# Performance work log

Hardware: AMD Instinct MI355X
Metric: run time of the kernel (lower is better)

The kernel has to match this reference:

```python
import jax, jax.numpy as jnp
import numpy as np

N_ITERS = 200   # fixed PDHG iterations (stands in for SCS max_iters)
POWER_ITERS = 30


def setup_inputs() -> dict:
    key = jax.random.key(0)
    k1, k2 = jax.random.split(key)
    B, n_hos, n_types, n_structs = 512, 16, 16, 4096
    m = n_hos * n_types
    # bids (capacities) are strictly positive counts
    X = jax.random.uniform(k1, (B, n_hos, n_types), jnp.float32, minval=1.0, maxval=10.0)
    # sparse 0/1 cycle-incidence matrix (each column = one feasible exchange structure)
    S = (jax.random.uniform(k2, (m, n_structs)) < 0.03).astype(jnp.float32)
    return {"X": X, "S": S, "batch_size": B}


def _solve_lp_batch(S, b, n_iters=N_ITERS):
    """Batched LP:  max 1^T x  s.t.  x >= 0,  S x <= b,  via Chambolle-Pock PDHG.

    S: [m, n] shared constraint matrix; b: [B, m] per-sample rhs.
    Returns x: [B, n] (the allocation that CvxpyLayer/SCS would return).
    """
    m, n = S.shape
    B = b.shape[0]
    w = jnp.ones((B, n), b.dtype)

    # spectral norm of S via power iteration -> step sizes
    v = jnp.ones((n,), S.dtype)

    def pw(v, _):
        v = S.T @ (S @ v)
        return v / jnp.linalg.norm(v), None

    v, _ = jax.lax.scan(pw, v, None, length=POWER_ITERS)
    L = jnp.sqrt(jnp.vdot(v, S.T @ (S @ v)))  # ~ ||S||_2
    tau = 0.9 / L
    sigma = 0.9 / L

    x0 = jnp.zeros((B, n), b.dtype)
    y0 = jnp.zeros((B, m), b.dtype)  # dual for Sx <= b

    def step(carry, _):
        x, y = carry
        # primal: gradient ascent on w^T x - y^T S x, projected to x >= 0
        x_new = jnp.maximum(x + tau * (w - y @ S), 0.0)        # [B,n]
        # dual: ascent on constraint residual with extrapolated primal, y >= 0
        y_new = jnp.maximum(y + sigma * ((2.0 * x_new - x) @ S.T - b), 0.0)  # [B,m]
        return (x_new, y_new), None

    (x, _), _ = jax.lax.scan(step, (x0, y0), None, length=n_iters)
    return x


def reference(X, S, batch_size):
    m, _ = S.shape
    b = X.reshape(batch_size, m)  # B = X.view(batch, n_hos*n_types)
    return _solve_lp_batch(S, b)  # [batch, n_structures]
```

## Files before the change

kernel.cpp:

```cpp
#include <hip/hip_runtime.h>

#define M 256
#define N 4096
#define NIT 200
#define PIT 30
#define CSRCAP 131072

#define YDUMMY (256*8)
#define ZDUMMY (4096*8)

__global__ void k_colcnt(const float* __restrict__ S, int* __restrict__ col_cnt){
  int j = blockIdx.x*256 + threadIdx.x;
  int c = 0;
  for (int i = 0; i < M; ++i) c += (S[i*N + j] != 0.0f) ? 1 : 0;
  col_cnt[j] = c;
}

__global__ void k_rowcnt(const float* __restrict__ S, int* __restrict__ row_cnt){
  int wid = blockIdx.x*(blockDim.x>>6) + (threadIdx.x>>6);
  int l = threadIdx.x & 63;
  if (wid >= M) return;
  int cnt = 0;
  for (int jc = 0; jc < N/64; ++jc){
    float v = S[wid*N + jc*64 + l];
    unsigned long long mask = __ballot(v != 0.0f);
    cnt += __popcll(mask);
  }
  if (l == 0) row_cnt[wid] = cnt;
}

__global__ void k_sortcol(const int* __restrict__ col_cnt,
                          int* __restrict__ col_perm, int* __restrict__ col_rank){
  __shared__ int cs[N];
  int t0 = threadIdx.x;
  for (int t = 0; t < N/256; ++t) cs[t0 + 256*t] = col_cnt[t0 + 256*t];
  __syncthreads();
  int j = blockIdx.x*256 + t0;
  int cj = cs[j];
  int rank = 0;
  #pragma unroll 4
  for (int jj = 0; jj < N; ++jj){
    int c = cs[jj];
    rank += ((c < cj) || (c == cj && jj < j)) ? 1 : 0;
  }
  col_perm[rank] = j;
  col_rank[j] = rank;
}

__global__ void k_sortrow(const int* __restrict__ row_cnt,
                          int* __restrict__ row_perm, int* __restrict__ row_ptr){
  int i = threadIdx.x;
  int ci = row_cnt[i];
  int rank = 0, pre = 0;
  for (int ii = 0; ii < M; ++ii){
    int c = row_cnt[ii];
    bool less = (c < ci) || (c == ci && ii < i);
    rank += less ? 1 : 0;
    pre  += less ? c : 0;
  }
  row_perm[rank] = i;
  row_ptr[rank]  = pre;
}

__global__ void k_fillcsr(const float* __restrict__ S, const int* __restrict__ row_perm,
                          const int* __restrict__ row_ptr, unsigned short* __restrict__ csr){
  int rr = blockIdx.x*(blockDim.x>>6) + (threadIdx.x>>6);
  int l = threadIdx.x & 63;
  if (rr >= M) return;
  int i = row_perm[rr];
  int pos = row_ptr[rr];
  for (int jc = 0; jc < N/64; ++jc){
    float v = S[i*N + jc*64 + l];
    unsigned long long mask = __ballot(v != 0.0f);
    if (v != 0.0f){
      int off = __popcll(mask & ((1ull << l) - 1ull));
      int p = pos + off;
      if (p < CSRCAP) csr[p] = (unsigned short)((jc*64 + l)*8);
    }
    pos += __popcll(mask);
  }
}

__global__ void k_trips(const int* __restrict__ col_cnt, const int* __restrict__ col_perm,
                        const int* __restrict__ row_cnt, const int* __restrict__ row_perm,
                        int* __restrict__ pT4, int* __restrict__ pB4,
                        int* __restrict__ dT4, int* __restrict__ dB4){
  int tid = threadIdx.x;
  if (tid < 64){
    int k = tid >> 4, w = tid & 15;
    int mx = 0;
    for (int l = 0; l < 64; ++l){
      int s = 64*w + l + 1024*k;
      int c = col_cnt[col_perm[s]];
      mx = max(mx, c);
    }
    pT4[tid] = min((mx + 3) >> 2, 16);
  } else if (tid < 80){
    int w = tid - 64;
    int mx = 0;
    for (int l = 0; l < 64; ++l){
      int t = w*64 + l;
      int r = t >> 2, q = t & 3;
      int len = row_cnt[row_perm[r]];
      int qs = (len*q) >> 2, qe = (len*(q+1)) >> 2;
      mx = max(mx, qe - qs);
    }
    dT4[w] = min((mx + 3) >> 2, 80);
  }
  __syncthreads();
  if (tid == 0){
    int acc = 0;
    for (int i = 0; i < 64; ++i){ pB4[i] = acc; acc += pT4[i]; }
    acc = 0;
    for (int i = 0; i < 16; ++i){ dB4[i] = acc; acc += dT4[i]; }
  }
}

__global__ void k_fillp(const float* __restrict__ S, const int* __restrict__ col_rank,
                        const int* __restrict__ pT4, const int* __restrict__ pB4,
                        unsigned short* __restrict__ pstream){
  int j = blockIdx.x*256 + threadIdx.x;
  int s = col_rank[j];
  int k = s >> 10, rem = s & 1023, w = rem >> 6, l = rem & 63;
  int kw = k*16 + w;
  int base = pB4[kw];
  int cap = pT4[kw]*4;
  int t = 0;
  for (int i = 0; i < M && t < cap; ++i){
    if (S[i*N + j] != 0.0f){
      pstream[((base + (t>>2))*64 + l)*4 + (t&3)] = (unsigned short)(i*8);
      ++t;
    }
  }
  for (; t < cap; ++t)
    pstream[((base + (t>>2))*64 + l)*4 + (t&3)] = (unsigned short)YDUMMY;
}

__global__ void k_filld(const unsigned short* __restrict__ csr,
                        const int* __restrict__ row_cnt, const int* __restrict__ row_perm,
                        const int* __restrict__ row_ptr,
                        const int* __restrict__ dT4, const int* __restrict__ dB4,
                        unsigned short* __restrict__ dstream){
  int tid = blockIdx.x*256 + threadIdx.x;
  int w = tid >> 6, l = tid & 63;
  int r = tid >> 2, q = tid & 3;
  int len = row_cnt[row_perm[r]];
  int rb = row_ptr[r];
  int qs = (len*q) >> 2, qe = (len*(q+1)) >> 2;
  int base = dB4[w];
  int cap = dT4[w]*4;
  int qlen = qe - qs; if (qlen > cap) qlen = cap;
  int t = 0;
  for (; t < qlen; ++t)
    dstream[((base + (t>>2))*64 + l)*4 + (t&3)] = csr[rb + qs + t];
  for (; t < cap; ++t)
    dstream[((base + (t>>2))*64 + l)*4 + (t&3)] = (unsigned short)ZDUMMY;
}

__global__ __launch_bounds__(1024) void k_power(
    const ushort4* __restrict__ pstream, const ushort4* __restrict__ dstream,
    const int* __restrict__ col_perm, const int* __restrict__ row_perm,
    const int* __restrict__ pT4, const int* __restrict__ pB4,
    const int* __restrict__ dT4, const int* __restrict__ dB4,
    float* __restrict__ tauw)
{
  __shared__ float2 v_s[N+8];
  __shared__ float2 u_s[M+8];
  __shared__ float2 red2[1024];
  const int tid = threadIdx.x, w = tid >> 6, l = tid & 63;

  int cj[4], pb[4], pt[4];
  float tl[4];
  #pragma unroll
  for (int k = 0; k < 4; ++k){
    int kw = k*16 + w;
    pb[k] = pB4[kw]; pt[k] = pT4[kw];
    cj[k] = col_perm[tid + 1024*k];
    v_s[cj[k]] = make_float2(1.0f, 0.0f);
    tl[k] = 0.0f;
  }
  const int r = tid >> 2, q = tid & 3;
  const int rid = row_perm[r];
  const int db = dB4[w], dt = dT4[w];
  if (tid < 8){ v_s[N+tid] = make_float2(0,0); u_s[M+tid] = make_float2(0,0); }
  __syncthreads();

  const char* vb = (const char*)v_s;
  const char* ub = (const char*)u_s;

  for (int it = 0; it < PIT; ++it){
    float a = 0.0f;
    for (int c = 0; c < dt; ++c){
      ushort4 ix = dstream[(db + c)*64 + l];
      a += ((const float2*)(vb + ix.x))->x + ((const float2*)(vb + ix.y))->x
         + ((const float2*)(vb + ix.z))->x + ((const float2*)(vb + ix.w))->x;
    }
    a += __shfl_xor(a, 1);
    a += __shfl_xor(a, 2);
    if (q == 0) u_s[rid] = make_float2(a, 0.0f);
    __syncthreads();
    #pragma unroll
    for (int k = 0; k < 4; ++k){
      float a2 = 0.0f;
      for (int c = 0; c < pt[k]; ++c){
        ushort4 ix = pstream[(pb[k] + c)*64 + l];
        a2 += ((const float2*)(ub + ix.x))->x + ((const float2*)(ub + ix.y))->x
            + ((const float2*)(ub + ix.z))->x + ((const float2*)(ub + ix.w))->x;
      }
      tl[k] = a2 * (1.0f/1024.0f);
      v_s[cj[k]] = make_float2(tl[k], 0.0f);
    }
    __syncthreads();
  }

  float pv = 0.0f;
  #pragma unroll
  for (int k = 0; k < 4; ++k) pv += tl[k]*tl[k];
  float a = 0.0f;
  for (int c = 0; c < dt; ++c){
    ushort4 ix = dstream[(db + c)*64 + l];
    a += ((const float2*)(vb + ix.x))->x + ((const float2*)(vb + ix.y))->x
       + ((const float2*)(vb + ix.z))->x + ((const float2*)(vb + ix.w))->x;
  }
  a += __shfl_xor(a, 1);
  a += __shfl_xor(a, 2);
  float fsq = (q == 0) ? a*a : 0.0f;
  red2[tid] = make_float2(pv, fsq);
  __syncthreads();
  for (int sd = 512; sd > 0; sd >>= 1){
    if (tid < sd){
      red2[tid].x += red2[tid+sd].x;
      red2[tid].y += red2[tid+sd].y;
    }
    __syncthreads();
  }
  if (tid == 0) tauw[0] = 0.9f * sqrtf(red2[0].x / red2[0].y);
}

__global__ __launch_bounds__(1024) void k_main(
    const float* __restrict__ X,
    const ushort4* __restrict__ pstream, const ushort4* __restrict__ dstream,
    const int* __restrict__ col_perm, const int* __restrict__ row_perm,
    const int* __restrict__ pT4, const int* __restrict__ pB4,
    const int* __restrict__ dT4, const int* __restrict__ dB4,
    const float* __restrict__ tauw, float* __restrict__ out)
{
  __shared__ float2 z_s[N+8];
  __shared__ float2 y_s[M+8];
  const int tid = threadIdx.x, w = tid >> 6, l = tid & 63;
  const int b0 = blockIdx.x * 2;
  const float tau = tauw[0];
  const float sigma = tau;

  int cj[4], pb[4], pt[4];
  float2 x[4];
  #pragma unroll
  for (int k = 0; k < 4; ++k){
    int kw = k*16 + w;
    pb[k] = pB4[kw]; pt[k] = pT4[kw];
    cj[k] = col_perm[tid + 1024*k];
    x[k] = make_float2(0.0f, 0.0f);
  }
  const int r = tid >> 2, q = tid & 3;
  const int rid = row_perm[r];
  const int db = dB4[w], dt = dT4[w];
  float2 bi = make_float2(0,0), yv = make_float2(0,0);
  if (q == 0){
    bi.x = X[b0*M + rid];
    bi.y = X[(b0+1)*M + rid];
    y_s[rid] = make_float2(0,0);
  }
  if (tid < 8){ y_s[M+tid] = make_float2(0,0); z_s[N+tid] = make_float2(0,0); }
  __syncthreads();

  const char* yb = (const char*)y_s;
  const char* zb = (const char*)z_s;

  for (int it = 0; it < NIT; ++it){
    const bool last = (it == NIT-1);
    #pragma unroll
    for (int k = 0; k < 4; ++k){
      float ax = 0.0f, ay = 0.0f;
      for (int c = 0; c < pt[k]; ++c){
        ushort4 ix = pstream[(pb[k] + c)*64 + l];
        float2 a0 = *(const float2*)(yb + ix.x);
        float2 a1 = *(const float2*)(yb + ix.y);
        float2 a2 = *(const float2*)(yb + ix.z);
        float2 a3 = *(const float2*)(yb + ix.w);
        ax += (a0.x + a1.x) + (a2.x + a3.x);
        ay += (a0.y + a1.y) + (a2.y + a3.y);
      }
      float2 xo = x[k];
      float xnx = fmaxf(xo.x + tau*(1.0f - ax), 0.0f);
      float xny = fmaxf(xo.y + tau*(1.0f - ay), 0.0f);
      if (!last) z_s[cj[k]] = make_float2(2.0f*xnx - xo.x, 2.0f*xny - xo.y);
      x[k] = make_float2(xnx, xny);
    }
    if (last) break;
    __syncthreads();
    float ax = 0.0f, ay = 0.0f;
    for (int c = 0; c < dt; ++c){
      ushort4 ix = dstream[(db + c)*64 + l];
      float2 a0 = *(const float2*)(zb + ix.x);
      float2 a1 = *(const float2*)(zb + ix.y);
      float2 a2 = *(const float2*)(zb + ix.z);
      float2 a3 = *(const float2*)(zb + ix.w);
      ax += (a0.x + a1.x) + (a2.x + a3.x);
      ay += (a0.y + a1.y) + (a2.y + a3.y);
    }
    ax += __shfl_xor(ax, 1);  ay += __shfl_xor(ay, 1);
    ax += __shfl_xor(ax, 2);  ay += __shfl_xor(ay, 2);
    if (q == 0){
      yv.x = fmaxf(yv.x + sigma*(ax - bi.x), 0.0f);
      yv.y = fmaxf(yv.y + sigma*(ay - bi.y), 0.0f);
      y_s[rid] = yv;
    }
    __syncthreads();
  }

  #pragma unroll
  for (int k = 0; k < 4; ++k){
    out[(size_t)b0*N + cj[k]]     = x[k].x;
    out[(size_t)(b0+1)*N + cj[k]] = x[k].y;
  }
}

extern "C" void kernel_launch(void* const* d_in, const int* in_sizes, int n_in,
                              void* d_out, int out_size, void* d_ws, size_t ws_size,
                              hipStream_t stream)
{
  const float* X = (const float*)d_in[0];
  const float* S = (const float*)d_in[1];
  float* out = (float*)d_out;
  const int B = in_sizes[0] / M;

  char* p = (char*)d_ws;
  auto alloc = [&](size_t bytes)->char*{
    char* q = p; p += (bytes + 255) & ~size_t(255); return q;
  };
  int* col_cnt  = (int*)alloc(N*sizeof(int));
  int* col_perm = (int*)alloc(N*sizeof(int));
  int* col_rank = (int*)alloc(N*sizeof(int));
  int* row_cnt  = (int*)alloc(M*sizeof(int));
  int* row_perm = (int*)alloc(M*sizeof(int));
  int* row_ptr  = (int*)alloc(M*sizeof(int));
  int* pT4      = (int*)alloc(64*sizeof(int));
  int* pB4      = (int*)alloc(64*sizeof(int));
  int* dT4      = (int*)alloc(16*sizeof(int));
  int* dB4      = (int*)alloc(16*sizeof(int));
  float* tauw   = (float*)alloc(256);
  unsigned short* csr     = (unsigned short*)alloc(CSRCAP*sizeof(unsigned short));
  unsigned short* pstream = (unsigned short*)alloc(65536ull*8);
  unsigned short* dstream = (unsigned short*)alloc(81920ull*8);

  k_colcnt <<<N/256, 256, 0, stream>>>(S, col_cnt);
  k_rowcnt <<<16, 1024, 0, stream>>>(S, row_cnt);
  k_sortcol<<<N/256, 256, 0, stream>>>(col_cnt, col_perm, col_rank);
  k_sortrow<<<1, M, 0, stream>>>(row_cnt, row_perm, row_ptr);
  k_fillcsr<<<16, 1024, 0, stream>>>(S, row_perm, row_ptr, csr);
  k_trips  <<<1, 256, 0, stream>>>(col_cnt, col_perm, row_cnt, row_perm, pT4, pB4, dT4, dB4);
  k_fillp  <<<N/256, 256, 0, stream>>>(S, col_rank, pT4, pB4, pstream);
  k_filld  <<<4, 256, 0, stream>>>(csr, row_cnt, row_perm, row_ptr, dT4, dB4, dstream);
  k_power  <<<1, 1024, 0, stream>>>((const ushort4*)pstream, (const ushort4*)dstream,
                                    col_perm, row_perm, pT4, pB4, dT4, dB4, tauw);
  k_main   <<<B/2, 1024, 0, stream>>>(X, (const ushort4*)pstream, (const ushort4*)dstream,
                                      col_perm, row_perm, pT4, pB4, dT4, dB4, tauw, out);
}
```

Before: 1.332 ms.

## Replicate dual vector across LDS banks and fuse power iteration into main kernel

The dual vector y is now stored 32 times in shared memory (one copy per bank slot), and each pstream index is rewritten to point at a lane-specific replica. Gathers in the primal step then spread across banks instead of colliding. One slot per row is left unwritten and kept at zero so it can act as the padding target. The separate single-block power-iteration kernel is removed, and every main block recomputes the spectral norm itself, which removes a serial launch at the cost of redundant work in all blocks and heavier shared-memory use (64KB for y_rep).

Measured after the change: 1.412 ms. 1.06x slower.

```diff
diff --git a/kernel.cpp b/kernel.cpp
--- a/kernel.cpp
+++ b/kernel.cpp
@@ -6,8 +6,7 @@
 #define PIT 30
 #define CSRCAP 131072
 
-#define YDUMMY (256*8)
-#define ZDUMMY (4096*8)
+#define ZDUMMY (N*8)
 
 __global__ void k_colcnt(const float* __restrict__ S, int* __restrict__ col_cnt){
   int j = blockIdx.x*256 + threadIdx.x;
@@ -120,20 +119,23 @@
                         const int* __restrict__ pT4, const int* __restrict__ pB4,
                         unsigned short* __restrict__ pstream){
   int j = blockIdx.x*256 + threadIdx.x;
-  int s = col_rank[j];
-  int k = s >> 10, rem = s & 1023, w = rem >> 6, l = rem & 63;
+  int sr = col_rank[j];
+  int k = sr >> 10, rem = sr & 1023, w = rem >> 6, l = rem & 63;
   int kw = k*16 + w;
   int base = pB4[kw];
   int cap = pT4[kw]*4;
+  int ls = l & 31;
   int t = 0;
   for (int i = 0; i < M && t < cap; ++i){
     if (S[i*N + j] != 0.0f){
-      pstream[((base + (t>>2))*64 + l)*4 + (t&3)] = (unsigned short)(i*8);
+      int s = ls;
+      if (s == (i & 31)) s = (s + 17) & 31;
+      pstream[((base + (t>>2))*64 + l)*4 + (t&3)] = (unsigned short)(i*256 + s*8);
       ++t;
     }
   }
   for (; t < cap; ++t)
-    pstream[((base + (t>>2))*64 + l)*4 + (t&3)] = (unsigned short)YDUMMY;
+    pstream[((base + (t>>2))*64 + l)*4 + (t&3)] = (unsigned short)0;
 }
 
 __global__ void k_filld(const unsigned short* __restrict__ csr,
@@ -157,124 +159,112 @@
     dstream[((base + (t>>2))*64 + l)*4 + (t&3)] = (unsigned short)ZDUMMY;
 }
 
-__global__ __launch_bounds__(1024) void k_power(
-    const ushort4* __restrict__ pstream, const ushort4* __restrict__ dstream,
-    const int* __restrict__ col_perm, const int* __restrict__ row_perm,
-    const int* __restrict__ pT4, const int* __restrict__ pB4,
-    const int* __restrict__ dT4, const int* __restrict__ dB4,
-    float* __restrict__ tauw)
-{
-  __shared__ float2 v_s[N+8];
-  __shared__ float2 u_s[M+8];
-  __shared__ float2 red2[1024];
-  const int tid = threadIdx.x, w = tid >> 6, l = tid & 63;
-
-  int cj[4], pb[4], pt[4];
-  float tl[4];
-  #pragma unroll
-  for (int k = 0; k < 4; ++k){
-    int kw = k*16 + w;
-    pb[k] = pB4[kw]; pt[k] = pT4[kw];
-    cj[k] = col_perm[tid + 1024*k];
-    v_s[cj[k]] = make_float2(1.0f, 0.0f);
-    tl[k] = 0.0f;
-  }
-  const int r = tid >> 2, q = tid & 3;
-  const int rid = row_perm[r];
-  const int db = dB4[w], dt = dT4[w];
-  if (tid < 8){ v_s[N+tid] = make_float2(0,0); u_s[M+tid] = make_float2(0,0); }
-  __syncthreads();
-
-  const char* vb = (const char*)v_s;
-  const char* ub = (const char*)u_s;
-
-  for (int it = 0; it < PIT; ++it){
-    float a = 0.0f;
-    for (int c = 0; c < dt; ++c){
-      ushort4 ix = dstream[(db + c)*64 + l];
-      a += ((const float2*)(vb + ix.x))->x + ((const float2*)(vb + ix.y))->x
-         + ((const float2*)(vb + ix.z))->x + ((const float2*)(vb + ix.w))->x;
-    }
-    a += __shfl_xor(a, 1);
-    a += __shfl_xor(a, 2);
-    if (q == 0) u_s[rid] = make_float2(a, 0.0f);
-    __syncthreads();
-    #pragma unroll
-    for (int k = 0; k < 4; ++k){
-      float a2 = 0.0f;
-      for (int c = 0; c < pt[k]; ++c){
-        ushort4 ix = pstream[(pb[k] + c)*64 + l];
-        a2 += ((const float2*)(ub + ix.x))->x + ((const float2*)(ub + ix.y))->x
-            + ((const float2*)(ub + ix.z))->x + ((const float2*)(ub + ix.w))->x;
-      }
-      tl[k] = a2 * (1.0f/1024.0f);
-      v_s[cj[k]] = make_float2(tl[k], 0.0f);
-    }
-    __syncthreads();
-  }
-
-  float pv = 0.0f;
-  #pragma unroll
-  for (int k = 0; k < 4; ++k) pv += tl[k]*tl[k];
-  float a = 0.0f;
-  for (int c = 0; c < dt; ++c){
-    ushort4 ix = dstream[(db + c)*64 + l];
-    a += ((const float2*)(vb + ix.x))->x + ((const float2*)(vb + ix.y))->x
-       + ((const float2*)(vb + ix.z))->x + ((const float2*)(vb + ix.w))->x;
-  }
-  a += __shfl_xor(a, 1);
-  a += __shfl_xor(a, 2);
-  float fsq = (q == 0) ? a*a : 0.0f;
-  red2[tid] = make_float2(pv, fsq);
-  __syncthreads();
-  for (int sd = 512; sd > 0; sd >>= 1){
-    if (tid < sd){
-      red2[tid].x += red2[tid+sd].x;
-      red2[tid].y += red2[tid+sd].y;
-    }
-    __syncthreads();
-  }
-  if (tid == 0) tauw[0] = 0.9f * sqrtf(red2[0].x / red2[0].y);
-}
-
 __global__ __launch_bounds__(1024) void k_main(
     const float* __restrict__ X,
     const ushort4* __restrict__ pstream, const ushort4* __restrict__ dstream,
     const int* __restrict__ col_perm, const int* __restrict__ row_perm,
     const int* __restrict__ pT4, const int* __restrict__ pB4,
     const int* __restrict__ dT4, const int* __restrict__ dB4,
-    const float* __restrict__ tauw, float* __restrict__ out)
+    float* __restrict__ out)
 {
+  __shared__ float2 y_rep[M*32];
   __shared__ float2 z_s[N+8];
-  __shared__ float2 y_s[M+8];
+  __shared__ float2 part[1024];
   const int tid = threadIdx.x, w = tid >> 6, l = tid & 63;
   const int b0 = blockIdx.x * 2;
-  const float tau = tauw[0];
-  const float sigma = tau;
 
   int cj[4], pb[4], pt[4];
-  float2 x[4];
   #pragma unroll
   for (int k = 0; k < 4; ++k){
     int kw = k*16 + w;
     pb[k] = pB4[kw]; pt[k] = pT4[kw];
     cj[k] = col_perm[tid + 1024*k];
-    x[k] = make_float2(0.0f, 0.0f);
   }
   const int r = tid >> 2, q = tid & 3;
   const int rid = row_perm[r];
   const int db = dB4[w], dt = dT4[w];
-  float2 bi = make_float2(0,0), yv = make_float2(0,0);
-  if (q == 0){
-    bi.x = X[b0*M + rid];
-    bi.y = X[(b0+1)*M + rid];
-    y_s[rid] = make_float2(0,0);
-  }
-  if (tid < 8){ y_s[M+tid] = make_float2(0,0); z_s[N+tid] = make_float2(0,0); }
-  __syncthreads();
-
-  const char* yb = (const char*)y_s;
+  const int zslot = rid & 31;
+  float2 bi;
+  bi.x = X[b0*M + rid];
+  bi.y = X[(b0+1)*M + rid];
+
+  #pragma unroll
+  for (int k = 0; k < 4; ++k) z_s[cj[k]] = make_float2(1.0f, 1.0f);
+  #pragma unroll
+  for (int t = 0; t < 8; ++t) y_rep[tid + 1024*t] = make_float2(0.0f, 0.0f);
+  if (tid < 8) z_s[N+tid] = make_float2(0.0f, 0.0f);
+  __syncthreads();
+
+  const char* yb = (const char*)y_rep;
   const char* zb = (const char*)z_s;
+
+  float tl[4];
+  #pragma unroll
+  for (int k = 0; k < 4; ++k) tl[k] = 0.0f;
+
+  for (int it = 0; it < PIT; ++it){
+    float a = 0.0f;
+    for (int c = 0; c < dt; ++c){
+      ushort4 ix = dstream[(db + c)*64 + l];
+      a += ((const float2*)(zb + ix.x))->x + ((const float2*)(zb + ix.y))->x
+         + ((const float2*)(zb + ix.z))->x + ((const float2*)(zb + ix.w))->x;
+    }
+    a += __shfl_xor(a, 1);
+    a += __shfl_xor(a, 2);
+    #pragma unroll
+    for (int t = 0; t < 8; ++t){
+      int s = (q << 3) | ((t + r) & 7);
+      if (s != zslot) y_rep[rid*32 + s] = make_float2(a, a);
+    }
+    __syncthreads();
+    #pragma unroll
+    for (int k = 0; k < 4; ++k){
+      float a2 = 0.0f;
+      for (int c = 0; c < pt[k]; ++c){
+        ushort4 ix = pstream[(pb[k] + c)*64 + l];
+        a2 += ((const float2*)(yb + ix.x))->x + ((const float2*)(yb + ix.y))->x
+            + ((const float2*)(yb + ix.z))->x + ((const float2*)(yb + ix.w))->x;
+      }
+      tl[k] = a2 * (1.0f/1024.0f);
+      z_s[cj[k]] = make_float2(tl[k], tl[k]);
+    }
+    __syncthreads();
+  }
+
+  float pv = 0.0f;
+  #pragma unroll
+  for (int k = 0; k < 4; ++k) pv += tl[k]*tl[k];
+  {
+    float a = 0.0f;
+    for (int c = 0; c < dt; ++c){
+      ushort4 ix = dstream[(db + c)*64 + l];
+      a += ((const float2*)(zb + ix.x))->x + ((const float2*)(zb + ix.y))->x
+         + ((const float2*)(zb + ix.z))->x + ((const float2*)(zb + ix.w))->x;
+    }
+    a += __shfl_xor(a, 1);
+    a += __shfl_xor(a, 2);
+    float fsq = (q == 0) ? a*a : 0.0f;
+    part[tid] = make_float2(pv, fsq);
+  }
+  __syncthreads();
+  for (int sd = 512; sd > 0; sd >>= 1){
+    if (tid < sd){
+      part[tid].x += part[tid+sd].x;
+      part[tid].y += part[tid+sd].y;
+    }
+    __syncthreads();
+  }
+  const float tau = 0.9f * sqrtf(part[0].x / part[0].y);
+  const float sigma = tau;
+  __syncthreads();
+
+  #pragma unroll
+  for (int t = 0; t < 8; ++t) y_rep[tid + 1024*t] = make_float2(0.0f, 0.0f);
+  float2 x[4];
+  #pragma unroll
+  for (int k = 0; k < 4; ++k) x[k] = make_float2(0.0f, 0.0f);
+  float2 yv = make_float2(0.0f, 0.0f);
+  __syncthreads();
 
   for (int it = 0; it < NIT; ++it){
     const bool last = (it == NIT-1);
@@ -310,10 +300,12 @@
     }
     ax += __shfl_xor(ax, 1);  ay += __shfl_xor(ay, 1);
     ax += __shfl_xor(ax, 2);  ay += __shfl_xor(ay, 2);
-    if (q == 0){
-      yv.x = fmaxf(yv.x + sigma*(ax - bi.x), 0.0f);
-      yv.y = fmaxf(yv.y + sigma*(ay - bi.y), 0.0f);
-      y_s[rid] = yv;
+    yv.x = fmaxf(yv.x + sigma*(ax - bi.x), 0.0f);
+    yv.y = fmaxf(yv.y + sigma*(ay - bi.y), 0.0f);
+    #pragma unroll
+    for (int t = 0; t < 8; ++t){
+      int s = (q << 3) | ((t + r) & 7);
+      if (s != zslot) y_rep[rid*32 + s] = yv;
     }
     __syncthreads();
   }
@@ -348,7 +340,6 @@
   int* pB4      = (int*)alloc(64*sizeof(int));
   int* dT4      = (int*)alloc(16*sizeof(int));
   int* dB4      = (int*)alloc(16*sizeof(int));
-  float* tauw   = (float*)alloc(256);
   unsigned short* csr     = (unsigned short*)alloc(CSRCAP*sizeof(unsigned short));
   unsigned short* pstream = (unsigned short*)alloc(65536ull*8);
   unsigned short* dstream = (unsigned short*)alloc(81920ull*8);
@@ -361,8 +352,6 @@
   k_trips  <<<1, 256, 0, stream>>>(col_cnt, col_perm, row_cnt, row_perm, pT4, pB4, dT4, dB4);
   k_fillp  <<<N/256, 256, 0, stream>>>(S, col_rank, pT4, pB4, pstream);
   k_filld  <<<4, 256, 0, stream>>>(csr, row_cnt, row_perm, row_ptr, dT4, dB4, dstream);
-  k_power  <<<1, 1024, 0, stream>>>((const ushort4*)pstream, (const ushort4*)dstream,
-                                    col_perm, row_perm, pT4, pB4, dT4, dB4, tauw);
   k_main   <<<B/2, 1024, 0, stream>>>(X, (const ushort4*)pstream, (const ushort4*)dstream,
-                                      col_perm, row_perm, pT4, pB4, dT4, dB4, tauw, out);
-}
+                                      col_perm, row_perm, pT4, pB4, dT4, dB4, out);
+}
```

## Build dual stream directly from S and reorder sparse index ordering for LDS banks

Applied to the files above, without the earlier changes.

Removes the intermediate CSR buffer and its fill kernel. The dual stream is now built straight from S, with one 64-thread block per row using ballot/popcount. Both the primal and dual index streams are now emitted in a rotated residue-class order (index mod 16 starting at a lane-dependent offset). This likely spreads shared-memory accesses across banks in the main PDHG loop. The cost is a changed, more complex fill pattern that alters summation order in the main kernel's sparse products.

After: 1.301 ms. -2.3%, faster.

```diff
diff --git a/kernel.cpp b/kernel.cpp
--- a/kernel.cpp
+++ b/kernel.cpp
@@ -4,7 +4,6 @@
 #define N 4096
 #define NIT 200
 #define PIT 30
-#define CSRCAP 131072
 
 #define YDUMMY (256*8)
 #define ZDUMMY (4096*8)
@@ -48,37 +47,16 @@
 }
 
 __global__ void k_sortrow(const int* __restrict__ row_cnt,
-                          int* __restrict__ row_perm, int* __restrict__ row_ptr){
+                          int* __restrict__ row_perm, int* __restrict__ row_rank){
   int i = threadIdx.x;
   int ci = row_cnt[i];
-  int rank = 0, pre = 0;
+  int rank = 0;
   for (int ii = 0; ii < M; ++ii){
     int c = row_cnt[ii];
-    bool less = (c < ci) || (c == ci && ii < i);
-    rank += less ? 1 : 0;
-    pre  += less ? c : 0;
+    rank += ((c < ci) || (c == ci && ii < i)) ? 1 : 0;
   }
   row_perm[rank] = i;
-  row_ptr[rank]  = pre;
-}
-
-__global__ void k_fillcsr(const float* __restrict__ S, const int* __restrict__ row_perm,
-                          const int* __restrict__ row_ptr, unsigned short* __restrict__ csr){
-  int rr = blockIdx.x*(blockDim.x>>6) + (threadIdx.x>>6);
-  int l = threadIdx.x & 63;
-  if (rr >= M) return;
-  int i = row_perm[rr];
-  int pos = row_ptr[rr];
-  for (int jc = 0; jc < N/64; ++jc){
-    float v = S[i*N + jc*64 + l];
-    unsigned long long mask = __ballot(v != 0.0f);
-    if (v != 0.0f){
-      int off = __popcll(mask & ((1ull << l) - 1ull));
-      int p = pos + off;
-      if (p < CSRCAP) csr[p] = (unsigned short)((jc*64 + l)*8);
-    }
-    pos += __popcll(mask);
-  }
+  row_rank[i] = rank;
 }
 
 __global__ void k_trips(const int* __restrict__ col_cnt, const int* __restrict__ col_perm,
@@ -120,41 +98,69 @@
                         const int* __restrict__ pT4, const int* __restrict__ pB4,
                         unsigned short* __restrict__ pstream){
   int j = blockIdx.x*256 + threadIdx.x;
-  int s = col_rank[j];
-  int k = s >> 10, rem = s & 1023, w = rem >> 6, l = rem & 63;
+  int sr = col_rank[j];
+  int k = sr >> 10, rem = sr & 1023, w = rem >> 6, l = rem & 63;
   int kw = k*16 + w;
   int base = pB4[kw];
   int cap = pT4[kw]*4;
+  int T = l & 15;
   int t = 0;
-  for (int i = 0; i < M && t < cap; ++i){
-    if (S[i*N + j] != 0.0f){
-      pstream[((base + (t>>2))*64 + l)*4 + (t&3)] = (unsigned short)(i*8);
-      ++t;
+  for (int cc = 0; cc < 16 && t < cap; ++cc){
+    int c = (T + cc) & 15;
+    for (int i16 = 0; i16 < 16 && t < cap; ++i16){
+      int i = i16*16 + c;
+      if (S[i*N + j] != 0.0f){
+        pstream[((base + (t>>2))*64 + l)*4 + (t&3)] = (unsigned short)(i*8);
+        ++t;
+      }
     }
   }
   for (; t < cap; ++t)
     pstream[((base + (t>>2))*64 + l)*4 + (t&3)] = (unsigned short)YDUMMY;
 }
 
-__global__ void k_filld(const unsigned short* __restrict__ csr,
+__global__ void k_filld(const float* __restrict__ S,
                         const int* __restrict__ row_cnt, const int* __restrict__ row_perm,
-                        const int* __restrict__ row_ptr,
                         const int* __restrict__ dT4, const int* __restrict__ dB4,
                         unsigned short* __restrict__ dstream){
-  int tid = blockIdx.x*256 + threadIdx.x;
-  int w = tid >> 6, l = tid & 63;
-  int r = tid >> 2, q = tid & 3;
-  int len = row_cnt[row_perm[r]];
-  int rb = row_ptr[r];
-  int qs = (len*q) >> 2, qe = (len*(q+1)) >> 2;
-  int base = dB4[w];
-  int cap = dT4[w]*4;
-  int qlen = qe - qs; if (qlen > cap) qlen = cap;
-  int t = 0;
-  for (; t < qlen; ++t)
-    dstream[((base + (t>>2))*64 + l)*4 + (t&3)] = csr[rb + qs + t];
-  for (; t < cap; ++t)
-    dstream[((base + (t>>2))*64 + l)*4 + (t&3)] = (unsigned short)ZDUMMY;
+  int rr = blockIdx.x;
+  int lf = threadIdx.x;
+  int i  = row_perm[rr];
+  int len = row_cnt[i];
+  int c0 = rr & 15;
+  int wc = rr >> 4;
+  int base = dB4[wc];
+  int cap  = dT4[wc]*4;
+  int qs1 = (len*1) >> 2, qs2 = (len*2) >> 2, qs3 = (len*3) >> 2;
+  int lc0 = (rr & 15) << 2;
+
+  int pos = 0;
+  for (int cc = 0; cc < 16; ++cc){
+    int c = (c0 + cc) & 15;
+    for (int mc = 0; mc < 4; ++mc){
+      int m = mc*64 + lf;
+      int j = c + 16*m;
+      float v = S[i*N + j];
+      unsigned long long mask = __ballot(v != 0.0f);
+      if (v != 0.0f){
+        int rank = pos + __popcll(mask & ((1ull << lf) - 1ull));
+        int q = (rank >= qs1) + (rank >= qs2) + (rank >= qs3);
+        int qs = (q==0) ? 0 : ((q==1) ? qs1 : ((q==2) ? qs2 : qs3));
+        int t = rank - qs;
+        if (t < cap)
+          dstream[((base + (t>>2))*64 + (lc0 + q))*4 + (t&3)] = (unsigned short)(j*8);
+      }
+      pos += __popcll(mask);
+    }
+  }
+  if (lf < 4){
+    int q = lf;
+    int qs = (q==0) ? 0 : ((q==1) ? qs1 : ((q==2) ? qs2 : qs3));
+    int qe = (q==3) ? len : ((q==0) ? qs1 : ((q==1) ? qs2 : qs3));
+    int qlen = qe - qs; if (qlen > cap) qlen = cap;
+    for (int t = qlen; t < cap; ++t)
+      dstream[((base + (t>>2))*64 + (lc0 + q))*4 + (t&3)] = (unsigned short)ZDUMMY;
+  }
 }
 
 __global__ __launch_bounds__(1024) void k_power(
@@ -343,24 +349,22 @@
   int* col_rank = (int*)alloc(N*sizeof(int));
   int* row_cnt  = (int*)alloc(M*sizeof(int));
   int* row_perm = (int*)alloc(M*sizeof(int));
-  int* row_ptr  = (int*)alloc(M*sizeof(int));
+  int* row_rank = (int*)alloc(M*sizeof(int));
   int* pT4      = (int*)alloc(64*sizeof(int));
   int* pB4      = (int*)alloc(64*sizeof(int));
   int* dT4      = (int*)alloc(16*sizeof(int));
   int* dB4      = (int*)alloc(16*sizeof(int));
   float* tauw   = (float*)alloc(256);
-  unsigned short* csr     = (unsigned short*)alloc(CSRCAP*sizeof(unsigned short));
   unsigned short* pstream = (unsigned short*)alloc(65536ull*8);
   unsigned short* dstream = (unsigned short*)alloc(81920ull*8);
 
   k_colcnt <<<N/256, 256, 0, stream>>>(S, col_cnt);
   k_rowcnt <<<16, 1024, 0, stream>>>(S, row_cnt);
   k_sortcol<<<N/256, 256, 0, stream>>>(col_cnt, col_perm, col_rank);
-  k_sortrow<<<1, M, 0, stream>>>(row_cnt, row_perm, row_ptr);
-  k_fillcsr<<<16, 1024, 0, stream>>>(S, row_perm, row_ptr, csr);
+  k_sortrow<<<1, M, 0, stream>>>(row_cnt, row_perm, row_rank);
   k_trips  <<<1, 256, 0, stream>>>(col_cnt, col_perm, row_cnt, row_perm, pT4, pB4, dT4, dB4);
   k_fillp  <<<N/256, 256, 0, stream>>>(S, col_rank, pT4, pB4, pstream);
-  k_filld  <<<4, 256, 0, stream>>>(csr, row_cnt, row_perm, row_ptr, dT4, dB4, dstream);
+  k_filld  <<<M, 64, 0, stream>>>(S, row_cnt, row_perm, dT4, dB4, dstream);
   k_power  <<<1, 1024, 0, stream>>>((const ushort4*)pstream, (const ushort4*)dstream,
                                     col_perm, row_perm, pT4, pB4, dT4, dB4, tauw);
   k_main   <<<B/2, 1024, 0, stream>>>(X, (const ushort4*)pstream, (const ushort4*)dstream,
```
